# Optimization experiments

Hardware: AMD Instinct MI355X
Metric: run time of the kernel (lower is better)

Reference implementation:

```python
import jax, jax.numpy as jnp
import numpy as np

D_MODEL = 1024
N_HEADS = 16
D_FF = 2 * D_MODEL
EPS = 1e-6


def setup_inputs() -> dict:
    key = jax.random.key(0)
    ks = jax.random.split(key, 12)
    B, S, D = 2, 2048, D_MODEL
    w = lambda k, shape: (jax.random.normal(k, shape, dtype=jnp.float32) * 0.02)
    return {
        "x": jax.random.normal(ks[0], (B, S, D), dtype=jnp.float32),
        "mask": jnp.ones((B, S, S), dtype=jnp.int32),
        "alpha1": jnp.ones((D,), jnp.float32),
        "bias1": jnp.zeros((D,), jnp.float32),
        "Wq": w(ks[1], (D, D)), "bq": jnp.zeros((D,), jnp.float32),
        "Wk": w(ks[2], (D, D)), "bk": jnp.zeros((D,), jnp.float32),
        "Wv": w(ks[3], (D, D)), "bv": jnp.zeros((D,), jnp.float32),
        "Wo": w(ks[4], (D, D)), "bo": jnp.zeros((D,), jnp.float32),
        "alpha2": jnp.ones((D,), jnp.float32),
        "bias2": jnp.zeros((D,), jnp.float32),
        "W1": w(ks[5], (D, D_FF)), "b1": jnp.zeros((D_FF,), jnp.float32),
        "W2": w(ks[6], (D_FF, D)), "b2": jnp.zeros((D,), jnp.float32),
    }


def _norm(x, alpha, bias):
    # torch: alpha*(x-mean)/(std+eps)+bias, std is unbiased (ddof=1)
    mu = jnp.mean(x, axis=-1, keepdims=True)
    sd = jnp.std(x, axis=-1, ddof=1, keepdims=True)
    return alpha * (x - mu) / (sd + EPS) + bias


def _gelu(x):
    return jax.nn.gelu(x, approximate=False)  # torch F.gelu exact


def _attention(x2, mask, Wq, bq, Wk, bk, Wv, bv, Wo, bo):
    B, S, D = x2.shape
    h, dk = N_HEADS, D // N_HEADS
    # project and split heads: [B, h, S, dk]
    q = (x2 @ Wq + bq).reshape(B, S, h, dk).transpose(0, 2, 1, 3)
    k = (x2 @ Wk + bk).reshape(B, S, h, dk).transpose(0, 2, 1, 3)
    v = (x2 @ Wv + bv).reshape(B, S, h, dk).transpose(0, 2, 1, 3)
    scores = jnp.einsum('bhqd,bhkd->bhqk', q, k) / np.sqrt(dk).astype(np.float32)
    scores = jnp.where(mask[:, None] == 0, jnp.float32(-1e9), scores)
    attn = jax.nn.softmax(scores, axis=-1)
    out = jnp.einsum('bhqk,bhkd->bhqd', attn, v)
    out = out.transpose(0, 2, 1, 3).reshape(B, S, D)
    return out @ Wo + bo


def reference(x, mask, alpha1, bias1, Wq, bq, Wk, bk, Wv, bv, Wo, bo,
              alpha2, bias2, W1, b1, W2, b2):
    x2 = _norm(x, alpha1, bias1)
    x = x + _attention(x2, mask, Wq, bq, Wk, bk, Wv, bv, Wo, bo)
    x2 = _norm(x, alpha2, bias2)
    ff = _gelu(_gelu(x2 @ W1 + b1) @ W2 + b2)
    return x + ff
```

## Files before the change

### kernel.cpp

```cpp
#include <hip/hip_runtime.h>
#include <math.h>

typedef __attribute__((ext_vector_type(8))) short v8s;
typedef __attribute__((ext_vector_type(4))) float v4f;
typedef __attribute__((ext_vector_type(4))) unsigned int v4u;
typedef __attribute__((ext_vector_type(2))) unsigned int v2u;

#define MFMA16(a,b,c) __builtin_amdgcn_mfma_f32_16x16x32_bf16(a,b,c,0,0,0)
#define QSCALE 0.18033688011112042f

typedef const __attribute__((address_space(1))) void* gp1_t;
typedef __attribute__((address_space(3))) void* lp3_t;
__device__ __forceinline__ void gll16(const void* g, void* l){
  __builtin_amdgcn_global_load_lds((gp1_t)g, (lp3_t)l, 16, 0, 0);
}

__device__ __forceinline__ unsigned short f2b(float f){
  unsigned u = __builtin_bit_cast(unsigned, f);
  u += 0x7FFFu + ((u>>16)&1u);
  return (unsigned short)(u>>16);
}
__device__ __forceinline__ unsigned cvtpk(float lo, float hi){
  unsigned r;
  asm("v_cvt_pk_bf16_f32 %0, %1, %2" : "=v"(r) : "v"(lo), "v"(hi));
  return r;
}
__device__ __forceinline__ float gelu_exact(float x){
  return 0.5f*x*(1.0f + erff(x*0.70710678118654752f));
}

__global__ __launch_bounds__(256) void ln_kernel(const float* __restrict__ x,
    const float* __restrict__ alpha, const float* __restrict__ bias,
    unsigned short* __restrict__ out)
{
  const int D = 1024;
  int row = blockIdx.x;
  int tid = threadIdx.x;
  const float* xr = x + (size_t)row*D;
  v4f v = ((const v4f*)xr)[tid];
  float s  = v[0]+v[1]+v[2]+v[3];
  float s2 = v[0]*v[0]+v[1]*v[1]+v[2]*v[2]+v[3]*v[3];
  #pragma unroll
  for (int off=1; off<64; off<<=1){ s += __shfl_xor(s, off); s2 += __shfl_xor(s2, off); }
  __shared__ float red[8];
  int w = tid>>6;
  if ((tid&63)==0){ red[w]=s; red[4+w]=s2; }
  __syncthreads();
  s  = red[0]+red[1]+red[2]+red[3];
  s2 = red[4]+red[5]+red[6]+red[7];
  float mu  = s*(1.0f/D);
  float var = (s2 - (float)D*mu*mu)*(1.0f/(D-1));
  float inv = 1.0f/(sqrtf(fmaxf(var,0.0f)) + 1e-6f);
  v4f a  = ((const v4f*)alpha)[tid];
  v4f bi = ((const v4f*)bias)[tid];
  unsigned short o[4];
  #pragma unroll
  for (int i=0;i<4;i++) o[i] = f2b(a[i]*(v[i]-mu)*inv + bi[i]);
  v2u pk; pk[0] = (unsigned)o[0] | ((unsigned)o[1]<<16);
          pk[1] = (unsigned)o[2] | ((unsigned)o[3]<<16);
  ((v2u*)(out + (size_t)row*D))[tid] = pk;
}

__global__ __launch_bounds__(256) void transpose_f2b(const float* __restrict__ in,
    unsigned short* __restrict__ out, int K, int N)
{
  __shared__ float t[32][33];
  int n0 = blockIdx.x*32, k0 = blockIdx.y*32;
  int tx = threadIdx.x, ty = threadIdx.y;
  #pragma unroll
  for (int j=0;j<4;j++) t[ty+8*j][tx] = in[(size_t)(k0+ty+8*j)*N + n0+tx];
  __syncthreads();
  #pragma unroll
  for (int j=0;j<4;j++) out[(size_t)(n0+ty+8*j)*K + k0+tx] = f2b(t[tx][ty+8*j]);
}

__global__ __launch_bounds__(256) void mask_flags(const int* __restrict__ mask,
    unsigned char* __restrict__ flags)
{
  const int S = 2048;
  int bid = blockIdx.x;
  int kt = bid & 31, qt = (bid>>5)&31, b = bid>>10;
  int tid = threadIdx.x;
  const int* mp = mask + (size_t)b*S*S + (size_t)(qt*64)*S + kt*64;
  int ok = 1;
  #pragma unroll
  for (int i=0;i<16;i++){
    int idx = tid + i*256;
    int row = idx>>6, col = idx&63;
    ok &= (mp[(size_t)row*S + col] != 0);
  }
  ok = __all(ok) ? 1 : 0;
  __shared__ int f[4];
  if ((tid&63)==0) f[tid>>6] = ok;
  __syncthreads();
  if (tid==0) flags[bid] = (unsigned char)(f[0]&f[1]&f[2]&f[3]);
}

__global__ __launch_bounds__(256) void v_transpose(const unsigned short* __restrict__ vB,
    unsigned short* __restrict__ vT)
{
  __shared__ unsigned short ts[64][68];
  int tt = blockIdx.x & 31, bh = blockIdx.x >> 5;
  int b = bh >> 4, h = bh & 15;
  int tid = threadIdx.x;
  int row = tid>>3, c8 = (tid&7)*8;
  const unsigned short* src = vB + ((size_t)(b*2048 + tt*64))*1024 + h*64;
  #pragma unroll
  for (int j=0;j<2;j++)
    *(v4u*)&ts[row+32*j][c8] = *(const v4u*)(src + (size_t)(row+32*j)*1024 + c8);
  __syncthreads();
  unsigned short* dst = vT + ((size_t)bh*64)*2048 + (size_t)tt*64;
  #pragma unroll
  for (int j=0;j<2;j++){
    int d = row + 32*j;
    unsigned short tmp[8];
    #pragma unroll
    for (int jj=0;jj<8;jj++) tmp[jj] = ts[c8+jj][d];
    *(v4u*)&dst[(size_t)d*2048 + c8] = *(const v4u*)tmp;
  }
}

__global__ __launch_bounds__(256) void gemm_qkv(
    const unsigned short* __restrict__ A, const unsigned short* __restrict__ Bt,
    const float* __restrict__ bq, const float* __restrict__ bk, const float* __restrict__ bv,
    unsigned short* __restrict__ qB, unsigned short* __restrict__ kB, unsigned short* __restrict__ vB)
{
  const int K = 1024, N = 1024;
  __shared__ unsigned short As[2][128][32];
  __shared__ unsigned short Bs[2][128][32];
  int m0 = blockIdx.x*128;
  int ny = blockIdx.y;
  int seg = ny>>3;
  int n0g = ny*128;
  int tid = threadIdx.x;
  int w = tid>>6, l = tid&63;
  int wm = (w>>1)*64, wn = (w&1)*64;
  int r16 = l&15, kq = l>>4;
  v4f acc[4][4] = {};
  int t4 = tid>>2, c8 = (tid&3)*8;
  const unsigned short* Ag = A  + (size_t)(m0 + t4)*K + c8;
  const unsigned short* Bg = Bt + (size_t)(n0g + t4)*K + c8;
  auto stageG = [&](int kb, int idx){
    char* a = (char*)&As[idx][0][0] + w*1024;
    char* b = (char*)&Bs[idx][0][0] + w*1024;
    gll16(Ag + kb,                a);
    gll16(Ag + (size_t)64*K + kb, a + 4096);
    gll16(Bg + kb,                b);
    gll16(Bg + (size_t)64*K + kb, b + 4096);
  };
  stageG(0, 0);
  for (int i=0; i<K/32; i++){
    int cur = i&1;
    __syncthreads();
    if (i+1 < K/32) stageG((i+1)*32, cur^1);
    v8s a[4], b[4];
    #pragma unroll
    for (int mi=0;mi<4;mi++) a[mi] = *(const v8s*)&As[cur][wm+mi*16+r16][kq*8];
    #pragma unroll
    for (int ni=0;ni<4;ni++) b[ni] = *(const v8s*)&Bs[cur][wn+ni*16+r16][kq*8];
    #pragma unroll
    for (int mi=0;mi<4;mi++)
      #pragma unroll
      for (int ni=0;ni<4;ni++)
        acc[mi][ni] = MFMA16(a[mi], b[ni], acc[mi][ni]);
  }
  unsigned short* ob = (seg==0) ? qB : (seg==1) ? kB : vB;
  const float*    bp = (seg==0) ? bq : (seg==1) ? bk : bv;
  float sc = (seg==0) ? QSCALE : 1.0f;
  int ncol0 = (ny&7)*128;
  #pragma unroll
  for (int mi=0;mi<4;mi++){
    #pragma unroll
    for (int ni=0;ni<4;ni++){
      int col = ncol0 + wn + ni*16 + r16;
      float bvv = bp[col];
      #pragma unroll
      for (int r=0;r<4;r++){
        int row = m0 + wm + mi*16 + kq*4 + r;
        ob[(size_t)row*N + col] = f2b((acc[mi][ni][r] + bvv)*sc);
      }
    }
  }
}

template<int MODE>
__global__ __launch_bounds__(256) void gemm_bt(
    const unsigned short* __restrict__ A, const unsigned short* __restrict__ Bt,
    const float* __restrict__ bias, const float* __restrict__ res,
    unsigned short* __restrict__ outb, float* __restrict__ outf,
    int M, int N, int K)
{
  __shared__ unsigned short As[2][128][32];
  __shared__ unsigned short Bs[2][128][32];
  int m0 = blockIdx.x*128, n0 = blockIdx.y*128;
  int tid = threadIdx.x;
  int w = tid>>6, l = tid&63;
  int wm = (w>>1)*64, wn = (w&1)*64;
  int r16 = l&15, kq = l>>4;
  v4f acc[4][4] = {};
  int t4 = tid>>2, c8 = (tid&3)*8;
  const unsigned short* Ag = A  + (size_t)(m0 + t4)*K + c8;
  const unsigned short* Bg = Bt + (size_t)(n0 + t4)*K + c8;
  auto stageG = [&](int kb, int idx){
    char* a = (char*)&As[idx][0][0] + w*1024;
    char* b = (char*)&Bs[idx][0][0] + w*1024;
    gll16(Ag + kb,                a);
    gll16(Ag + (size_t)64*K + kb, a + 4096);
    gll16(Bg + kb,                b);
    gll16(Bg + (size_t)64*K + kb, b + 4096);
  };
  stageG(0, 0);
  int nk = K/32;
  for (int i=0; i<nk; i++){
    int cur = i&1;
    __syncthreads();
    if (i+1 < nk) stageG((i+1)*32, cur^1);
    v8s a[4], b[4];
    #pragma unroll
    for (int mi=0;mi<4;mi++) a[mi] = *(const v8s*)&As[cur][wm+mi*16+r16][kq*8];
    #pragma unroll
    for (int ni=0;ni<4;ni++) b[ni] = *(const v8s*)&Bs[cur][wn+ni*16+r16][kq*8];
    #pragma unroll
    for (int mi=0;mi<4;mi++)
      #pragma unroll
      for (int ni=0;ni<4;ni++)
        acc[mi][ni] = MFMA16(a[mi], b[ni], acc[mi][ni]);
  }
  #pragma unroll
  for (int mi=0;mi<4;mi++){
    #pragma unroll
    for (int ni=0;ni<4;ni++){
      int col = n0 + wn + ni*16 + r16;
      float bv = bias[col];
      #pragma unroll
      for (int r=0;r<4;r++){
        int row = m0 + wm + mi*16 + kq*4 + r;
        float t = acc[mi][ni][r] + bv;
        if (MODE==2 || MODE==3) t = gelu_exact(t);
        if (MODE==2) outb[(size_t)row*N + col] = f2b(t);
        else         outf[(size_t)row*N + col] = t + res[(size_t)row*N + col];
      }
    }
  }
}

__global__ __launch_bounds__(256, 4) void attn_kernel(
    const unsigned short* __restrict__ Q, const unsigned short* __restrict__ Kb,
    const unsigned short* __restrict__ vT, const int* __restrict__ mask,
    const unsigned char* __restrict__ flags, unsigned short* __restrict__ out)
{
  const int S = 2048, D = 1024;
  __shared__ unsigned short Kb2[2][64][64];
  __shared__ unsigned short Vb2[2][64][64];
  __shared__ unsigned short Ps[4][16][36];
  int bid = (blockIdx.x & 7)*128 + (blockIdx.x >> 3);
  int qt = bid & 31;
  int bh = bid >> 5;
  int b = bh >> 4, h = bh & 15;
  int tid = threadIdx.x, w = tid>>6, l = tid&63;
  int r16 = l&15, kq = l>>4;
  const unsigned short* Qp  = Q  + (size_t)b*S*D + h*64;
  const unsigned short* Kp  = Kb + (size_t)b*S*D + h*64;
  const unsigned short* vTp = vT + (size_t)bh*64*S;
  int qrow0 = qt*64 + w*16;
  v8s qf[2];
  #pragma unroll
  for (int ks=0;ks<2;ks++)
    qf[ks] = *(const v8s*)(Qp + (size_t)(qrow0+r16)*D + ks*32 + kq*8);
  float m_run = -1e30f, l_run = 0.0f;
  v4f o[4] = {};
  const int* mp = mask + (size_t)b*S*S;
  const unsigned char* fl = flags + (size_t)(b*32 + qt)*32;

  int srow = l>>3;
  int gsw  = (l&7) ^ srow;
  auto stage = [&](int kt, int idx){
    int kt64 = kt*64;
    #pragma unroll
    for (int sub=0; sub<2; sub++){
      int row = w*16 + sub*8 + srow;
      gll16(Kp  + (size_t)(kt64+row)*D + gsw*8, &Kb2[idx][w*16+sub*8][0]);
      gll16(vTp + (size_t)row*S + kt64 + gsw*8, &Vb2[idx][w*16+sub*8][0]);
    }
  };

  stage(0, 0);
  for (int kt=0; kt<32; kt++){
    int cur = kt&1;
    __syncthreads();
    if (kt+1 < 32) stage(kt+1, cur^1);
    int kt64 = kt*64;
    int rx = r16 & 7;
    v4f s[4] = {};
    #pragma unroll
    for (int ks=0; ks<2; ks++){
      v8s kf[4];
      #pragma unroll
      for (int nj=0; nj<4; nj++)
        kf[nj] = *(const v8s*)&Kb2[cur][nj*16+r16][((ks*4+kq)^rx)*8];
      #pragma unroll
      for (int nj=0; nj<4; nj++)
        s[nj] = MFMA16(kf[nj], qf[ks], s[nj]);
    }
    if (!fl[kt]){
      int qrow = qrow0 + r16;
      #pragma unroll
      for (int nj=0;nj<4;nj++){
        #pragma unroll
        for (int r=0;r<4;r++){
          int kcol = kt64 + nj*16 + kq*4 + r;
          if (mp[(size_t)qrow*S + kcol] == 0) s[nj][r] = -3.0e38f;
        }
      }
    }
    float t0 = fmaxf(fmaxf(s[0][0],s[0][1]), fmaxf(s[0][2],s[0][3]));
    float t1 = fmaxf(fmaxf(s[1][0],s[1][1]), fmaxf(s[1][2],s[1][3]));
    float t2 = fmaxf(fmaxf(s[2][0],s[2][1]), fmaxf(s[2][2],s[2][3]));
    float t3 = fmaxf(fmaxf(s[3][0],s[3][1]), fmaxf(s[3][2],s[3][3]));
    float tm = fmaxf(fmaxf(t0,t1), fmaxf(t2,t3));
    tm = fmaxf(tm, __shfl_xor(tm,16));
    tm = fmaxf(tm, __shfl_xor(tm,32));
    if (!__all(tm <= m_run + 11.5f)){
      float mn = fmaxf(m_run, tm);
      float corr = exp2f(m_run - mn);
      m_run = mn;
      l_run *= corr;
      #pragma unroll
      for (int nj=0;nj<4;nj++)
        #pragma unroll
        for (int r=0;r<4;r++) o[nj][r] *= corr;
    }
    #pragma unroll
    for (int nj=0;nj<4;nj++)
      #pragma unroll
      for (int r=0;r<4;r++)
        s[nj][r] = exp2f(s[nj][r] - m_run);
    float a0 = (s[0][0]+s[0][1]) + (s[0][2]+s[0][3]);
    float a1 = (s[1][0]+s[1][1]) + (s[1][2]+s[1][3]);
    float a2 = (s[2][0]+s[2][1]) + (s[2][2]+s[2][3]);
    float a3 = (s[3][0]+s[3][1]) + (s[3][2]+s[3][3]);
    float rs = (a0+a1) + (a2+a3);
    rs += __shfl_xor(rs,16);
    rs += __shfl_xor(rs,32);
    l_run += rs;
    #pragma unroll
    for (int hh=0; hh<2; hh++){
      #pragma unroll
      for (int nj=hh*2; nj<hh*2+2; nj++){
        *(unsigned*)&Ps[w][r16][(nj&1)*16 + kq*4    ] = cvtpk(s[nj][0], s[nj][1]);
        *(unsigned*)&Ps[w][r16][(nj&1)*16 + kq*4 + 2] = cvtpk(s[nj][2], s[nj][3]);
      }
      v8s pa = *(const v8s*)&Ps[w][r16][kq*8];
      v8s vv[4];
      #pragma unroll
      for (int nj=0;nj<4;nj++)
        vv[nj] = *(const v8s*)&Vb2[cur][nj*16+r16][((hh*4+kq)^rx)*8];
      #pragma unroll
      for (int nj=0;nj<4;nj++)
        o[nj] = MFMA16(vv[nj], pa, o[nj]);
    }
  }
  float invl = 1.0f / l_run;
  size_t orow = (size_t)(b*S + qrow0 + r16)*D + h*64;
  #pragma unroll
  for (int nj=0;nj<4;nj++){
    v2u pk;
    pk[0] = cvtpk(o[nj][0]*invl, o[nj][1]*invl);
    pk[1] = cvtpk(o[nj][2]*invl, o[nj][3]*invl);
    *(v2u*)(out + orow + nj*16 + kq*4) = pk;
  }
}

extern "C" void kernel_launch(void* const* d_in, const int* in_sizes, int n_in,
                              void* d_out, int out_size, void* d_ws, size_t ws_size,
                              hipStream_t stream)
{
  const int D=1024, DFF=2048, BS=4096;
  const float* x      = (const float*)d_in[0];
  const int*   mask   = (const int*)d_in[1];
  const float* alpha1 = (const float*)d_in[2];
  const float* bias1  = (const float*)d_in[3];
  const float* Wq     = (const float*)d_in[4];
  const float* bq     = (const float*)d_in[5];
  const float* Wk     = (const float*)d_in[6];
  const float* bk     = (const float*)d_in[7];
  const float* Wv     = (const float*)d_in[8];
  const float* bv     = (const float*)d_in[9];
  const float* Wo     = (const float*)d_in[10];
  const float* bo     = (const float*)d_in[11];
  const float* alpha2 = (const float*)d_in[12];
  const float* bias2  = (const float*)d_in[13];
  const float* W1     = (const float*)d_in[14];
  const float* b1     = (const float*)d_in[15];
  const float* W2     = (const float*)d_in[16];
  const float* b2     = (const float*)d_in[17];
  float* outp = (float*)d_out;

  char* ws = (char*)d_ws;
  size_t off = 0;
  auto alloc = [&](size_t bytes){ void* p = ws+off; off += (bytes+255)&~(size_t)255; return p; };
  unsigned short* x2b    = (unsigned short*)alloc((size_t)BS*D*2);
  unsigned short* qB     = (unsigned short*)alloc((size_t)BS*D*2);
  unsigned short* kB     = (unsigned short*)alloc((size_t)BS*D*2);
  unsigned short* vB     = (unsigned short*)alloc((size_t)BS*D*2);
  unsigned short* attnB  = (unsigned short*)alloc((size_t)BS*D*2);
  unsigned short* h1     = (unsigned short*)alloc((size_t)BS*DFF*2);
  float*          xres   = (float*)alloc((size_t)BS*D*4);
  unsigned short* wqkvT  = (unsigned short*)alloc((size_t)3*D*D*2);
  unsigned short* woT    = (unsigned short*)alloc((size_t)D*D*2);
  unsigned short* w1T    = (unsigned short*)alloc((size_t)D*DFF*2);
  unsigned short* w2T    = (unsigned short*)alloc((size_t)DFF*D*2);
  unsigned char*  flg    = (unsigned char*)alloc(2048);
  unsigned short* vTb    = x2b;

  dim3 tb(32,8);
  transpose_f2b<<<dim3(D/32,  D/32 ), tb, 0, stream>>>(Wq, wqkvT,           D, D);
  transpose_f2b<<<dim3(D/32,  D/32 ), tb, 0, stream>>>(Wk, wqkvT + D*D,     D, D);
  transpose_f2b<<<dim3(D/32,  D/32 ), tb, 0, stream>>>(Wv, wqkvT + 2*D*D,   D, D);
  transpose_f2b<<<dim3(D/32,  D/32 ), tb, 0, stream>>>(Wo, woT, D, D);
  transpose_f2b<<<dim3(DFF/32,D/32 ), tb, 0, stream>>>(W1, w1T, D, DFF);
  transpose_f2b<<<dim3(D/32,  DFF/32), tb, 0, stream>>>(W2, w2T, DFF, D);

  mask_flags<<<2048, 256, 0, stream>>>(mask, flg);
  ln_kernel<<<BS, 256, 0, stream>>>(x, alpha1, bias1, x2b);

  gemm_qkv<<<dim3(BS/128, 24), 256, 0, stream>>>(x2b, wqkvT, bq, bk, bv, qB, kB, vB);

  v_transpose<<<1024, 256, 0, stream>>>(vB, vTb);

  attn_kernel<<<1024, 256, 0, stream>>>(qB, kB, vTb, mask, flg, attnB);

  gemm_bt<1><<<dim3(BS/128, D/128), 256, 0, stream>>>(attnB, woT, bo, x, nullptr, xres, BS, D, D);

  ln_kernel<<<BS, 256, 0, stream>>>(xres, alpha2, bias2, x2b);

  gemm_bt<2><<<dim3(BS/128, DFF/128), 256, 0, stream>>>(x2b, w1T, b1, nullptr, h1, nullptr, BS, DFF, D);
  gemm_bt<3><<<dim3(BS/128, D/128), 256, 0, stream>>>(h1, w2T, b2, xres, nullptr, outp, BS, D, DFF);
}
```

Measured before the change: 272.1 us.

## Triple-buffer GEMM and attention loads, add 64-row GEMM, widen attention blocks

Switches the GEMM and attention main loops from double to triple buffering, with explicit vmcnt waits and a raw s_barrier so two tiles of global-to-LDS loads stay in flight. Adds a 64x128-tile GEMM variant for the N=1024 output projections, which doubles the block count on the 256-CU part. Attention now runs 512-thread blocks covering 128 query rows, with the mask-flag check merged across both 64-row tiles. The extra LDS per block may reduce occupancy, and the hand-counted vmcnt values must match the number of issued loads.

After: 259.3 us. 1.05x faster.

```diff
diff --git a/kernel.cpp b/kernel.cpp
--- a/kernel.cpp
+++ b/kernel.cpp
@@ -14,6 +14,7 @@
 __device__ __forceinline__ void gll16(const void* g, void* l){
   __builtin_amdgcn_global_load_lds((gp1_t)g, (lp3_t)l, 16, 0, 0);
 }
+#define VMCNT(n) asm volatile("s_waitcnt vmcnt(" #n ")" ::: "memory")
 
 __device__ __forceinline__ unsigned short f2b(float f){
   unsigned u = __builtin_bit_cast(unsigned, f);
@@ -126,8 +127,8 @@
     unsigned short* __restrict__ qB, unsigned short* __restrict__ kB, unsigned short* __restrict__ vB)
 {
   const int K = 1024, N = 1024;
-  __shared__ unsigned short As[2][128][32];
-  __shared__ unsigned short Bs[2][128][32];
+  __shared__ unsigned short As[3][128][32];
+  __shared__ unsigned short Bs[3][128][32];
   int m0 = blockIdx.x*128;
   int ny = blockIdx.y;
   int seg = ny>>3;
@@ -148,11 +149,13 @@
     gll16(Bg + kb,                b);
     gll16(Bg + (size_t)64*K + kb, b + 4096);
   };
-  stageG(0, 0);
-  for (int i=0; i<K/32; i++){
-    int cur = i&1;
-    __syncthreads();
-    if (i+1 < K/32) stageG((i+1)*32, cur^1);
+  const int nk = K/32;
+  stageG(0, 0); stageG(32, 1);
+  for (int i=0; i<nk; i++){
+    int cur = i%3;
+    if (i+1 < nk) VMCNT(4); else VMCNT(0);
+    __builtin_amdgcn_s_barrier();
+    if (i+2 < nk) stageG((i+2)*32, (i+2)%3);
     v8s a[4], b[4];
     #pragma unroll
     for (int mi=0;mi<4;mi++) a[mi] = *(const v8s*)&As[cur][wm+mi*16+r16][kq*8];
@@ -190,8 +193,8 @@
     unsigned short* __restrict__ outb, float* __restrict__ outf,
     int M, int N, int K)
 {
-  __shared__ unsigned short As[2][128][32];
-  __shared__ unsigned short Bs[2][128][32];
+  __shared__ unsigned short As[3][128][32];
+  __shared__ unsigned short Bs[3][128][32];
   int m0 = blockIdx.x*128, n0 = blockIdx.y*128;
   int tid = threadIdx.x;
   int w = tid>>6, l = tid&63;
@@ -209,12 +212,13 @@
     gll16(Bg + kb,                b);
     gll16(Bg + (size_t)64*K + kb, b + 4096);
   };
-  stageG(0, 0);
-  int nk = K/32;
+  const int nk = K/32;
+  stageG(0, 0); stageG(32, 1);
   for (int i=0; i<nk; i++){
-    int cur = i&1;
-    __syncthreads();
-    if (i+1 < nk) stageG((i+1)*32, cur^1);
+    int cur = i%3;
+    if (i+1 < nk) VMCNT(4); else VMCNT(0);
+    __builtin_amdgcn_s_barrier();
+    if (i+2 < nk) stageG((i+2)*32, (i+2)%3);
     v8s a[4], b[4];
     #pragma unroll
     for (int mi=0;mi<4;mi++) a[mi] = *(const v8s*)&As[cur][wm+mi*16+r16][kq*8];
@@ -236,7 +240,7 @@
       for (int r=0;r<4;r++){
         int row = m0 + wm + mi*16 + kq*4 + r;
         float t = acc[mi][ni][r] + bv;
-        if (MODE==2 || MODE==3) t = gelu_exact(t);
+        if (MODE==2) t = gelu_exact(t);
         if (MODE==2) outb[(size_t)row*N + col] = f2b(t);
         else         outf[(size_t)row*N + col] = t + res[(size_t)row*N + col];
       }
@@ -244,25 +248,84 @@
   }
 }
 
-__global__ __launch_bounds__(256, 4) void attn_kernel(
+template<int MODE>
+__global__ __launch_bounds__(256) void gemm64_bt(
+    const unsigned short* __restrict__ A, const unsigned short* __restrict__ Bt,
+    const float* __restrict__ bias, const float* __restrict__ res,
+    float* __restrict__ outf, int M, int N, int K)
+{
+  __shared__ unsigned short As[3][64][32];
+  __shared__ unsigned short Bs[3][128][32];
+  int m0 = blockIdx.x*64, n0 = blockIdx.y*128;
+  int tid = threadIdx.x;
+  int w = tid>>6, l = tid&63;
+  int wm = (w>>1)*32, wn = (w&1)*64;
+  int r16 = l&15, kq = l>>4;
+  v4f acc[2][4] = {};
+  int t4 = tid>>2, c8 = (tid&3)*8;
+  const unsigned short* Ag = A  + (size_t)(m0 + t4)*K + c8;
+  const unsigned short* Bg = Bt + (size_t)(n0 + t4)*K + c8;
+  auto stageG = [&](int kb, int idx){
+    char* a = (char*)&As[idx][0][0] + w*1024;
+    char* b = (char*)&Bs[idx][0][0] + w*1024;
+    gll16(Ag + kb,                a);
+    gll16(Bg + kb,                b);
+    gll16(Bg + (size_t)64*K + kb, b + 4096);
+  };
+  const int nk = K/32;
+  stageG(0, 0); stageG(32, 1);
+  for (int i=0; i<nk; i++){
+    int cur = i%3;
+    if (i+1 < nk) VMCNT(3); else VMCNT(0);
+    __builtin_amdgcn_s_barrier();
+    if (i+2 < nk) stageG((i+2)*32, (i+2)%3);
+    v8s a[2], b[4];
+    #pragma unroll
+    for (int mi=0;mi<2;mi++) a[mi] = *(const v8s*)&As[cur][wm+mi*16+r16][kq*8];
+    #pragma unroll
+    for (int ni=0;ni<4;ni++) b[ni] = *(const v8s*)&Bs[cur][wn+ni*16+r16][kq*8];
+    #pragma unroll
+    for (int mi=0;mi<2;mi++)
+      #pragma unroll
+      for (int ni=0;ni<4;ni++)
+        acc[mi][ni] = MFMA16(a[mi], b[ni], acc[mi][ni]);
+  }
+  #pragma unroll
+  for (int mi=0;mi<2;mi++){
+    #pragma unroll
+    for (int ni=0;ni<4;ni++){
+      int col = n0 + wn + ni*16 + r16;
+      float bv = bias[col];
+      #pragma unroll
+      for (int r=0;r<4;r++){
+        int row = m0 + wm + mi*16 + kq*4 + r;
+        float t = acc[mi][ni][r] + bv;
+        if (MODE==3) t = gelu_exact(t);
+        outf[(size_t)row*N + col] = t + res[(size_t)row*N + col];
+      }
+    }
+  }
+}
+
+__global__ __launch_bounds__(512, 4) void attn_kernel(
     const unsigned short* __restrict__ Q, const unsigned short* __restrict__ Kb,
     const unsigned short* __restrict__ vT, const int* __restrict__ mask,
     const unsigned char* __restrict__ flags, unsigned short* __restrict__ out)
 {
   const int S = 2048, D = 1024;
-  __shared__ unsigned short Kb2[2][64][64];
-  __shared__ unsigned short Vb2[2][64][64];
-  __shared__ unsigned short Ps[4][16][36];
-  int bid = (blockIdx.x & 7)*128 + (blockIdx.x >> 3);
-  int qt = bid & 31;
-  int bh = bid >> 5;
+  __shared__ unsigned short Kb3[3][64][64];
+  __shared__ unsigned short Vb3[3][64][64];
+  __shared__ unsigned short Ps[8][16][36];
+  int bid = (blockIdx.x & 7)*64 + (blockIdx.x >> 3);
+  int qt = bid & 15;
+  int bh = bid >> 4;
   int b = bh >> 4, h = bh & 15;
   int tid = threadIdx.x, w = tid>>6, l = tid&63;
   int r16 = l&15, kq = l>>4;
   const unsigned short* Qp  = Q  + (size_t)b*S*D + h*64;
   const unsigned short* Kp  = Kb + (size_t)b*S*D + h*64;
   const unsigned short* vTp = vT + (size_t)bh*64*S;
-  int qrow0 = qt*64 + w*16;
+  int qrow0 = qt*128 + w*16;
   v8s qf[2];
   #pragma unroll
   for (int ks=0;ks<2;ks++)
@@ -270,25 +333,23 @@
   float m_run = -1e30f, l_run = 0.0f;
   v4f o[4] = {};
   const int* mp = mask + (size_t)b*S*S;
-  const unsigned char* fl = flags + (size_t)(b*32 + qt)*32;
+  const unsigned char* fl = flags + ((size_t)b*32 + qt*2)*32;
 
   int srow = l>>3;
   int gsw  = (l&7) ^ srow;
   auto stage = [&](int kt, int idx){
     int kt64 = kt*64;
-    #pragma unroll
-    for (int sub=0; sub<2; sub++){
-      int row = w*16 + sub*8 + srow;
-      gll16(Kp  + (size_t)(kt64+row)*D + gsw*8, &Kb2[idx][w*16+sub*8][0]);
-      gll16(vTp + (size_t)row*S + kt64 + gsw*8, &Vb2[idx][w*16+sub*8][0]);
-    }
+    int row = w*8 + srow;
+    gll16(Kp  + (size_t)(kt64+row)*D + gsw*8, &Kb3[idx][w*8][0]);
+    gll16(vTp + (size_t)row*S + kt64 + gsw*8, &Vb3[idx][w*8][0]);
   };
 
-  stage(0, 0);
+  stage(0, 0); stage(1, 1);
   for (int kt=0; kt<32; kt++){
-    int cur = kt&1;
-    __syncthreads();
-    if (kt+1 < 32) stage(kt+1, cur^1);
+    int cur = kt%3;
+    if (kt+1 < 32) VMCNT(2); else VMCNT(0);
+    __builtin_amdgcn_s_barrier();
+    if (kt+2 < 32) stage(kt+2, (kt+2)%3);
     int kt64 = kt*64;
     int rx = r16 & 7;
     v4f s[4] = {};
@@ -297,12 +358,12 @@
       v8s kf[4];
       #pragma unroll
       for (int nj=0; nj<4; nj++)
-        kf[nj] = *(const v8s*)&Kb2[cur][nj*16+r16][((ks*4+kq)^rx)*8];
+        kf[nj] = *(const v8s*)&Kb3[cur][nj*16+r16][((ks*4+kq)^rx)*8];
       #pragma unroll
       for (int nj=0; nj<4; nj++)
         s[nj] = MFMA16(kf[nj], qf[ks], s[nj]);
     }
-    if (!fl[kt]){
+    if (!(fl[kt] & fl[32+kt])){
       int qrow = qrow0 + r16;
       #pragma unroll
       for (int nj=0;nj<4;nj++){
@@ -354,7 +415,7 @@
       v8s vv[4];
       #pragma unroll
       for (int nj=0;nj<4;nj++)
-        vv[nj] = *(const v8s*)&Vb2[cur][nj*16+r16][((hh*4+kq)^rx)*8];
+        vv[nj] = *(const v8s*)&Vb3[cur][nj*16+r16][((hh*4+kq)^rx)*8];
       #pragma unroll
       for (int nj=0;nj<4;nj++)
         o[nj] = MFMA16(vv[nj], pa, o[nj]);
@@ -428,12 +489,12 @@
 
   v_transpose<<<1024, 256, 0, stream>>>(vB, vTb);
 
-  attn_kernel<<<1024, 256, 0, stream>>>(qB, kB, vTb, mask, flg, attnB);
-
-  gemm_bt<1><<<dim3(BS/128, D/128), 256, 0, stream>>>(attnB, woT, bo, x, nullptr, xres, BS, D, D);
+  attn_kernel<<<512, 512, 0, stream>>>(qB, kB, vTb, mask, flg, attnB);
+
+  gemm64_bt<1><<<dim3(BS/64, D/128), 256, 0, stream>>>(attnB, woT, bo, x, xres, BS, D, D);
 
   ln_kernel<<<BS, 256, 0, stream>>>(xres, alpha2, bias2, x2b);
 
   gemm_bt<2><<<dim3(BS/128, DFF/128), 256, 0, stream>>>(x2b, w1T, b1, nullptr, h1, nullptr, BS, DFF, D);
-  gemm_bt<3><<<dim3(BS/128, D/128), 256, 0, stream>>>(h1, w2T, b2, xres, nullptr, outp, BS, D, DFF);
-}
+  gemm64_bt<3><<<dim3(BS/64, D/128), 256, 0, stream>>>(h1, w2T, b2, xres, outp, BS, D, DFF);
+}
```
